# Optimization experiments

Hardware: AMD Instinct MI355X
Metric: run time of the kernel (lower is better)

Reference implementation:

```python
import jax, jax.numpy as jnp
import numpy as np

B, SQ, SKV, D, H, DH, P = 8, 2048, 2048, 1024, 8, 128, 1024
LN_EPS = 1e-3  # keras LayerNormalization default


def _glorot(key, shape):
    fan_in, fan_out = shape[-2], shape[-1]
    lim = np.sqrt(6.0 / (fan_in + fan_out))
    return jax.random.uniform(key, shape, jnp.float32, -lim, lim)


def _layernorm(x, gamma, beta, eps=LN_EPS):
    mu = jnp.mean(x, axis=-1, keepdims=True)
    var = jnp.mean(jnp.square(x - mu), axis=-1, keepdims=True)
    return (x - mu) * jax.lax.rsqrt(var + eps) * gamma + beta


def setup_inputs() -> dict:
    key = jax.random.key(0)
    ks = jax.random.split(key, 8)
    return {
        "query": jax.random.normal(ks[0], (B, SQ, D), jnp.float32),
        "value": jax.random.normal(ks[1], (B, SKV, D), jnp.float32),
        "W1": _glorot(ks[2], (H, D, DH)),   # per-head query proj (stacked)
        "W2": _glorot(ks[3], (H, D, DH)),   # per-head key proj
        "W3": _glorot(ks[4], (H, D, DH)),   # per-head value proj
        "Wp": _glorot(ks[5], (H * DH, P)),  # output projection
        "bp": jnp.zeros((P,), jnp.float32),
        "Wt": _glorot(ks[6], (P, P)),       # transform (relu FFN)
        "bt": jnp.zeros((P,), jnp.float32),
        "g1": jnp.ones((P,), jnp.float32),
        "b1": jnp.zeros((P,), jnp.float32),
        "g2": jnp.ones((P,), jnp.float32),
        "b2": jnp.zeros((P,), jnp.float32),
    }


def reference(query, value, W1, W2, W3, Wp, bp, Wt, bt, g1, b1, g2, b2):
    # batched multi-head attention (original loops over heads; math identical)
    q = jnp.einsum("bsd,hde->bhse", query, W1)   # [B,H,SQ,DH]
    k = jnp.einsum("btd,hde->bhte", value, W2)   # [B,H,SKV,DH]
    v = jnp.einsum("btd,hde->bhte", value, W3)   # [B,H,SKV,DH]
    scale = 1.0 / jnp.sqrt(jnp.asarray(DH, jnp.float32))
    scores = jnp.einsum("bhse,bhte->bhst", q, k) * scale
    attn = jax.nn.softmax(scores, axis=-1)
    ctx = jnp.einsum("bhst,bhte->bhse", attn, v)  # [B,H,SQ,DH]
    # concat heads along feature axis
    cat = ctx.transpose(0, 2, 1, 3).reshape(B, SQ, H * DH)
    # project + residual + layernorm (dropout inactive: rate=0 / inference)
    proj = cat @ Wp + bp + query
    proj = _layernorm(proj, g1, b1)
    # relu transform + residual + layernorm
    t = jax.nn.relu(proj @ Wt + bt) + proj
    return _layernorm(t, g2, b2)
```

## Files before the change

### kernel.cpp

```cpp
#include <hip/hip_runtime.h>
#include <hip/hip_bf16.h>


typedef __bf16 bf16x8 __attribute__((ext_vector_type(8)));
typedef float  f32x4  __attribute__((ext_vector_type(4)));
typedef float  f32x16 __attribute__((ext_vector_type(16)));
typedef unsigned u32x4 __attribute__((ext_vector_type(4)));

#define GLDS16(g, l)                                                         \
  __builtin_amdgcn_global_load_lds(                                          \
      (__attribute__((address_space(1))) void*)(g),                          \
      (__attribute__((address_space(3))) void*)(l), 16, 0, 0)

__device__ __forceinline__ unsigned short f2bfu(float f) {
  unsigned int u = __builtin_bit_cast(unsigned int, f);
  u += 0x7fffu + ((u >> 16) & 1u);
  return (unsigned short)(u >> 16);
}
__device__ __forceinline__ float bfu2f(unsigned short u) {
  return __builtin_bit_cast(float, (unsigned int)u << 16);
}

__global__ __launch_bounds__(256) void cast2_f32_bf16(
    const float* __restrict__ in0, unsigned short* __restrict__ out0,
    const float* __restrict__ in1, unsigned short* __restrict__ out1, int n) {
  const float* in = blockIdx.z ? in1 : in0;
  unsigned short* out = blockIdx.z ? out1 : out0;
  int i = (blockIdx.x * 256 + threadIdx.x) * 4;
  int stride = gridDim.x * 256 * 4;
  for (; i < n; i += stride) {
    float4 v = *(const float4*)(in + i);
    ushort4 o;
    o.x = f2bfu(v.x); o.y = f2bfu(v.y); o.z = f2bfu(v.z); o.w = f2bfu(v.w);
    *(ushort4*)(out + i) = o;
  }
}

__device__ __forceinline__ void tc_body(const float* in, unsigned short* out,
                                        int R, int C) {
  __shared__ float tile[32][33];
  int tx = threadIdx.x, ty = threadIdx.y;
  int c0 = blockIdx.x * 32, r0 = blockIdx.y * 32;
#pragma unroll
  for (int j = 0; j < 4; j++)
    tile[ty + j * 8][tx] = in[(size_t)(r0 + ty + j * 8) * C + c0 + tx];
  __syncthreads();
#pragma unroll
  for (int j = 0; j < 4; j++)
    out[(size_t)(c0 + ty + j * 8) * R + r0 + tx] = f2bfu(tile[tx][ty + j * 8]);
}

__global__ __launch_bounds__(256) void transpose_all(
    const float* __restrict__ W1, const float* __restrict__ W2,
    const float* __restrict__ W3, const float* __restrict__ Wp,
    const float* __restrict__ Wt, unsigned short* __restrict__ O1,
    unsigned short* __restrict__ O2, unsigned short* __restrict__ O3,
    unsigned short* __restrict__ Op, unsigned short* __restrict__ Ot) {
  int z = blockIdx.z;
  if (z < 24) {
    if (blockIdx.x >= 4) return;
    int t = z >> 3, s = z & 7;
    const float* in = (t == 0 ? W1 : t == 1 ? W2 : W3) + (size_t)s * 1024 * 128;
    unsigned short* out = (t == 0 ? O1 : t == 1 ? O2 : O3) + (size_t)s * 1024 * 128;
    tc_body(in, out, 1024, 128);
  } else {
    const float* in = (z == 24) ? Wp : Wt;
    unsigned short* out = (z == 24) ? Op : Ot;
    tc_body(in, out, 1024, 1024);
  }
}

__device__ __forceinline__ void gemm128_core(
    const char* gA, const char* gB, char* lds, f32x4 (&acc)[4][4], int tid) {
  int wid = tid >> 6, lane = tid & 63;
  int l15 = lane & 15, l4 = lane >> 4;
  int wm = (wid >> 1) * 64, wn = (wid & 1) * 64;

  auto STAGE = [&](int buf, int t) {
    char* ab = lds + buf * 32768;
    char* bb = ab + 16384;
#pragma unroll
    for (int i = 0; i < 4; i++) {
      int s = i * 256 + tid;
      int row = s >> 3;
      int g = (s & 7) ^ (row & 7);
      unsigned dst = (unsigned)((i * 256 + (tid & ~63)) * 16);
      GLDS16(gA + (size_t)row * 2048 + t * 128 + g * 16, ab + dst);
      GLDS16(gB + (size_t)row * 2048 + t * 128 + g * 16, bb + dst);
    }
  };

  STAGE(0, 0);
  for (int t = 0; t < 16; t++) {
    __builtin_amdgcn_sched_barrier(0);
    __builtin_amdgcn_s_barrier();
    if (t < 15) {
      STAGE((t + 1) & 1, t + 1);
      asm volatile("s_waitcnt vmcnt(8)" ::: "memory");
    } else {
      asm volatile("s_waitcnt vmcnt(0)" ::: "memory");
    }
    __builtin_amdgcn_s_barrier();
    __builtin_amdgcn_sched_barrier(0);

    const char* ab = lds + (t & 1) * 32768;
    const char* bb = ab + 16384;
#pragma unroll
    for (int kk = 0; kk < 2; kk++) {
      bf16x8 af[4], bfr[4];
#pragma unroll
      for (int f = 0; f < 4; f++) {
        int ra = wm + f * 16 + l15;
        af[f] = *(const bf16x8*)(ab + ra * 128 + (((kk * 4 + l4) ^ (ra & 7)) << 4));
        int rb = wn + f * 16 + l15;
        bfr[f] = *(const bf16x8*)(bb + rb * 128 + (((kk * 4 + l4) ^ (rb & 7)) << 4));
      }
      __builtin_amdgcn_s_setprio(1);
#pragma unroll
      for (int mf = 0; mf < 4; mf++)
#pragma unroll
        for (int nf = 0; nf < 4; nf++)
          acc[mf][nf] = __builtin_amdgcn_mfma_f32_16x16x32_bf16(
              af[mf], bfr[nf], acc[mf][nf], 0, 0, 0);
      __builtin_amdgcn_s_setprio(0);
    }
  }
}

__global__ __launch_bounds__(256, 2) void gemm_qkv(
    const unsigned short* __restrict__ qbf, const unsigned short* __restrict__ vbf,
    const unsigned short* __restrict__ Wq_t, const unsigned short* __restrict__ Wk_t,
    const unsigned short* __restrict__ Wv_t, unsigned short* __restrict__ Qh,
    unsigned short* __restrict__ Kh, unsigned short* __restrict__ Vt,
    float qscale) {
  int nb = gridDim.x;
  int qq = nb >> 3;
  int lin = blockIdx.x;
  int idx = (lin & 7) * qq + (lin >> 3);

  const unsigned short *A, *Bt;
  unsigned short* outp;
  int m0, n0, mode;
  float sc = 1.0f;
  if (idx < 2048) {
    int seg = idx >> 10;
    int t = idx & 1023;
    m0 = (t >> 3) * 128; n0 = (t & 7) * 128;
    A = seg ? vbf : qbf;
    Bt = seg ? Wk_t : Wq_t;
    outp = seg ? Kh : Qh;
    if (!seg) sc = qscale;
    mode = 0;
  } else {
    int v = idx - 2048;
    int bz = v >> 7, t = v & 127;
    m0 = (t >> 4) * 128; n0 = (t & 15) * 128;
    A = Wv_t;
    Bt = vbf + (size_t)bz * 2048 * 1024;
    outp = Vt + (size_t)bz * 1024 * 2048;
    mode = 1;
  }

  __shared__ alignas(16) char lds[65536];
  f32x4 acc[4][4];
#pragma unroll
  for (int i = 0; i < 4; i++)
#pragma unroll
    for (int j = 0; j < 4; j++) acc[i][j] = (f32x4){0.f, 0.f, 0.f, 0.f};

  gemm128_core((const char*)A + (size_t)m0 * 2048,
               (const char*)Bt + (size_t)n0 * 2048, lds, acc, threadIdx.x);

  int tid = threadIdx.x, wid = tid >> 6, lane = tid & 63;
  int l15 = lane & 15, l4 = lane >> 4;
  int wm = (wid >> 1) * 64, wn = (wid & 1) * 64;
#pragma unroll
  for (int mf = 0; mf < 4; mf++)
#pragma unroll
    for (int nf = 0; nf < 4; nf++)
#pragma unroll
      for (int r = 0; r < 4; r++) {
        int gm = m0 + wm + mf * 16 + l4 * 4 + r;
        int gn = n0 + wn + nf * 16 + l15;
        float v = acc[mf][nf][r];
        if (mode == 0) {
          int b = gm >> 11, s = gm & 2047, h = gn >> 7, e = gn & 127;
          outp[((((size_t)b * 8 + h) * 2048 + s) << 7) + e] = f2bfu(v * sc);
        } else {
          outp[(size_t)gm * 2048 + gn] = f2bfu(v);
        }
      }
}

template <int MODE>
__global__ __launch_bounds__(256, 2) void gemm128_ep(
    const unsigned short* __restrict__ A, const unsigned short* __restrict__ Bt,
    unsigned short* __restrict__ out, const float* __restrict__ bias,
    const unsigned short* __restrict__ extra) {
  int nb = gridDim.x;
  int qq = nb >> 3;
  int lin = blockIdx.x;
  int idx = (lin & 7) * qq + (lin >> 3);
  int m0 = (idx >> 3) * 128, n0 = (idx & 7) * 128;

  __shared__ alignas(16) char lds[65536];
  f32x4 acc[4][4];
#pragma unroll
  for (int i = 0; i < 4; i++)
#pragma unroll
    for (int j = 0; j < 4; j++) acc[i][j] = (f32x4){0.f, 0.f, 0.f, 0.f};

  gemm128_core((const char*)A + (size_t)m0 * 2048,
               (const char*)Bt + (size_t)n0 * 2048, lds, acc, threadIdx.x);

  int tid = threadIdx.x, wid = tid >> 6, lane = tid & 63;
  int l15 = lane & 15, l4 = lane >> 4;
  int wm = (wid >> 1) * 64, wn = (wid & 1) * 64;
#pragma unroll
  for (int mf = 0; mf < 4; mf++)
#pragma unroll
    for (int nf = 0; nf < 4; nf++)
#pragma unroll
      for (int r = 0; r < 4; r++) {
        int gm = m0 + wm + mf * 16 + l4 * 4 + r;
        int gn = n0 + wn + nf * 16 + l15;
        float v = acc[mf][nf][r];
        float pl = bfu2f(extra[(size_t)gm * 1024 + gn]);
        if constexpr (MODE == 2)
          out[(size_t)gm * 1024 + gn] = f2bfu(v + bias[gn] + pl);
        else
          out[(size_t)gm * 1024 + gn] = f2bfu(fmaxf(v + bias[gn], 0.0f) + pl);
      }
}

__global__ __launch_bounds__(512) void fa_kernel(
    const unsigned short* __restrict__ Qh,
    const unsigned short* __restrict__ Kh,
    const unsigned short* __restrict__ Vt,
    unsigned short* __restrict__ catO) {
  int h = blockIdx.x, qt = blockIdx.y, b = blockIdx.z;
  int tid = threadIdx.x, wid = tid >> 6, lane = tid & 63;
  int q31 = lane & 31, hi = lane >> 5;

  __shared__ alignas(16) char lds[131072];

  const char* gK = (const char*)(Kh + (((size_t)b * 8 + h) * 2048) * 128);
  const char* gV = (const char*)(Vt + ((size_t)b * 1024 + h * 128) * 2048);

  bf16x8 qf[8];
  {
    const char* gQ = (const char*)(Qh + (((size_t)b * 8 + h) * 2048
                        + (size_t)qt * 256 + wid * 32 + q31) * 128);
#pragma unroll
    for (int ks = 0; ks < 8; ks++)
      qf[ks] = *(const bf16x8*)(gQ + ks * 32 + hi * 16);
  }

  f32x16 o[4];
#pragma unroll
  for (int et = 0; et < 4; et++)
#pragma unroll
    for (int r = 0; r < 16; r++) o[et][r] = 0.f;
  float lacc0 = 0.f, lacc1 = 0.f;

  auto STAGE_K = [&](int kt) {
    char* kb = lds + (kt & 3) * 16384;
#pragma unroll
    for (int pass = 0; pass < 2; pass++) {
      int c = pass * 512 + tid;
      int row = c >> 4, ch = c & 15;
      int g = ch ^ (row & 15);
      GLDS16(gK + (size_t)(kt * 64 + row) * 256 + g * 16,
             kb + (pass * 512 + (tid & ~63)) * 16);
    }
  };
  auto STAGE_V = [&](int kt) {
    char* vb = lds + 65536 + (kt & 3) * 16384;
#pragma unroll
    for (int pass = 0; pass < 2; pass++) {
      int c = pass * 512 + tid;
      int row = c >> 4, g = c & 15;
      int gp = g ^ (row & 15);
      int e = ((gp >> 3) << 6) + row;
      GLDS16(gV + (size_t)e * 4096 + kt * 128 + (gp & 7) * 16,
             vb + (pass * 512 + (tid & ~63)) * 16);
    }
  };
  auto QK = [&](int kt, f32x16& r0, f32x16& r1) {
    const char* kb = lds + (kt & 3) * 16384;
#pragma unroll
    for (int r = 0; r < 16; r++) { r0[r] = 0.f; r1[r] = 0.f; }
#pragma unroll
    for (int ks = 0; ks < 8; ks++) {
      int g = ((2 * ks + hi) ^ (q31 & 15)) << 4;
      bf16x8 k0 = *(const bf16x8*)(kb + q31 * 256 + g);
      bf16x8 k1 = *(const bf16x8*)(kb + (q31 + 32) * 256 + g);
      r0 = __builtin_amdgcn_mfma_f32_32x32x16_bf16(k0, qf[ks], r0, 0, 0, 0);
      r1 = __builtin_amdgcn_mfma_f32_32x32x16_bf16(k1, qf[ks], r1, 0, 0, 0);
    }
  };
  auto SOFT_PV = [&](int kt, f32x16& s0, f32x16& s1) {
    float p[32];
#pragma unroll
    for (int r = 0; r < 16; r++) p[r] = __builtin_amdgcn_exp2f(s0[r]);
#pragma unroll
    for (int r = 0; r < 16; r++) p[16 + r] = __builtin_amdgcn_exp2f(s1[r]);
#pragma unroll
    for (int r = 0; r < 16; r++) { lacc0 += p[r]; lacc1 += p[16 + r]; }
    bf16x8 pa[4];
#pragma unroll
    for (int g = 0; g < 4; g++) {
      unsigned a0, a1, b0, b1;
      float p0 = p[g * 8 + 0], p1 = p[g * 8 + 1], p2 = p[g * 8 + 2], p3 = p[g * 8 + 3];
      float p4 = p[g * 8 + 4], p5 = p[g * 8 + 5], p6 = p[g * 8 + 6], p7 = p[g * 8 + 7];
      asm("v_cvt_pk_bf16_f32 %0, %1, %2" : "=v"(a0) : "v"(p0), "v"(p1));
      asm("v_cvt_pk_bf16_f32 %0, %1, %2" : "=v"(b0) : "v"(p4), "v"(p5));
      asm("v_cvt_pk_bf16_f32 %0, %1, %2" : "=v"(a1) : "v"(p2), "v"(p3));
      asm("v_cvt_pk_bf16_f32 %0, %1, %2" : "=v"(b1) : "v"(p6), "v"(p7));
      asm volatile("v_permlane32_swap_b32 %0, %1" : "+v"(a0), "+v"(b0));
      asm volatile("v_permlane32_swap_b32 %0, %1" : "+v"(a1), "+v"(b1));
      u32x4 w; w[0] = a0; w[1] = a1; w[2] = b0; w[3] = b1;
      pa[g] = __builtin_bit_cast(bf16x8, w);
    }
    const char* vb = lds + 65536 + (kt & 3) * 16384;
#pragma unroll
    for (int et = 0; et < 4; et++) {
      int row = (et & 1) * 32 + q31;
      int gb = (et >> 1) * 8;
#pragma unroll
      for (int ks = 0; ks < 4; ks++) {
        bf16x8 vf = *(const bf16x8*)(vb + row * 256 +
                        (((gb + 2 * ks + hi) ^ (row & 15)) << 4));
        o[et] = __builtin_amdgcn_mfma_f32_32x32x16_bf16(vf, pa[ks], o[et], 0, 0, 0);
      }
    }
  };

  STAGE_K(0); STAGE_V(0); STAGE_K(1); STAGE_V(1);

  for (int w = 0; w < 16; w++) {
    int kt = 2 * w;
    asm volatile("s_waitcnt lgkmcnt(0)" ::: "memory");
    __builtin_amdgcn_sched_barrier(0);
    __builtin_amdgcn_s_barrier();
    if (w < 15) {
      STAGE_K(kt + 2); STAGE_V(kt + 2); STAGE_K(kt + 3); STAGE_V(kt + 3);
      asm volatile("s_waitcnt vmcnt(8)" ::: "memory");
    } else {
      asm volatile("s_waitcnt vmcnt(0)" ::: "memory");
    }
    __builtin_amdgcn_s_barrier();
    __builtin_amdgcn_sched_barrier(0);
    f32x16 sA0, sA1, sB0, sB1;
    QK(kt, sA0, sA1);
    QK(kt + 1, sB0, sB1);
    SOFT_PV(kt, sA0, sA1);
    SOFT_PV(kt + 1, sB0, sB1);
  }

  float lacc = lacc0 + lacc1;
  lacc += __shfl_xor(lacc, 32);
  float linv = 1.0f / lacc;
  __syncthreads();
  char* reg = lds + wid * 8192;
  int swz = (lane & 7) << 4;
#pragma unroll
  for (int et = 0; et < 4; et++)
#pragma unroll
    for (int pr = 0; pr < 8; pr++) {
      float lo = o[et][2 * pr] * linv, hf = o[et][2 * pr + 1] * linv;
      unsigned w;
      asm("v_cvt_pk_bf16_f32 %0, %1, %2" : "=v"(w) : "v"(lo), "v"(hf));
      int e = et * 32 + 8 * (pr >> 1) + 4 * hi + (pr & 1) * 2;
      *(unsigned*)(reg + q31 * 256 + ((e * 2) ^ swz)) = w;
    }
  size_t orow = (size_t)b * 2048 + (size_t)qt * 256 + wid * 32;
#pragma unroll
  for (int pass = 0; pass < 8; pass++) {
    int n = pass * 64 + lane;
    int q = n >> 4, ch = n & 15;
    bf16x8 v = *(const bf16x8*)(reg + q * 256 + ((ch * 16) ^ ((q & 7) << 4)));
    *(bf16x8*)((char*)(catO + (orow + q) * 1024 + h * 128) + ch * 16) = v;
  }
}

template <int IN_BF16, int OUT_BF16>
__global__ __launch_bounds__(256) void ln_kernel(
    const void* __restrict__ in, const float* __restrict__ g,
    const float* __restrict__ be, void* __restrict__ out) {
  int row = blockIdx.x;
  int tid = threadIdx.x;
  float4 v;
  if constexpr (IN_BF16) {
    ushort4 u = ((const ushort4*)in)[(size_t)row * 256 + tid];
    v.x = bfu2f(u.x); v.y = bfu2f(u.y); v.z = bfu2f(u.z); v.w = bfu2f(u.w);
  } else {
    v = ((const float4*)in)[(size_t)row * 256 + tid];
  }
  float s = v.x + v.y + v.z + v.w;
  float sq = v.x * v.x + v.y * v.y + v.z * v.z + v.w * v.w;
#pragma unroll
  for (int m = 1; m < 64; m <<= 1) {
    s += __shfl_xor(s, m);
    sq += __shfl_xor(sq, m);
  }
  __shared__ float ws[8];
  int wid = tid >> 6, lane = tid & 63;
  if (lane == 0) { ws[wid] = s; ws[wid + 4] = sq; }
  __syncthreads();
  s = ws[0] + ws[1] + ws[2] + ws[3];
  sq = ws[4] + ws[5] + ws[6] + ws[7];
  float mu = s * (1.0f / 1024.0f);
  float var = sq * (1.0f / 1024.0f) - mu * mu;
  float rs = rsqrtf(var + 1e-3f);
  float4 gg = ((const float4*)g)[tid];
  float4 bb = ((const float4*)be)[tid];
  float y0 = (v.x - mu) * rs * gg.x + bb.x;
  float y1 = (v.y - mu) * rs * gg.y + bb.y;
  float y2 = (v.z - mu) * rs * gg.z + bb.z;
  float y3 = (v.w - mu) * rs * gg.w + bb.w;
  if constexpr (OUT_BF16) {
    ushort4 ov;
    ov.x = f2bfu(y0); ov.y = f2bfu(y1); ov.z = f2bfu(y2); ov.w = f2bfu(y3);
    ((ushort4*)out)[(size_t)row * 256 + tid] = ov;
  } else {
    float4 ov = {y0, y1, y2, y3};
    ((float4*)out)[(size_t)row * 256 + tid] = ov;
  }
}

extern "C" void kernel_launch(void* const* d_in, const int* in_sizes, int n_in,
                              void* d_out, int out_size, void* d_ws, size_t ws_size,
                              hipStream_t stream) {
  const float* query = (const float*)d_in[0];
  const float* value = (const float*)d_in[1];
  const float* W1 = (const float*)d_in[2];
  const float* W2 = (const float*)d_in[3];
  const float* W3 = (const float*)d_in[4];
  const float* Wp = (const float*)d_in[5];
  const float* bp = (const float*)d_in[6];
  const float* Wt = (const float*)d_in[7];
  const float* bt = (const float*)d_in[8];
  const float* g1 = (const float*)d_in[9];
  const float* b1 = (const float*)d_in[10];
  const float* g2 = (const float*)d_in[11];
  const float* b2 = (const float*)d_in[12];

  char* ws = (char*)d_ws;
  unsigned short* qbf  = (unsigned short*)(ws + 0);
  unsigned short* vbf  = (unsigned short*)(ws + 33554432);
  unsigned short* Qh   = (unsigned short*)(ws + 67108864);
  unsigned short* Kh   = (unsigned short*)(ws + 100663296);
  unsigned short* Vt   = (unsigned short*)(ws + 134217728);
  unsigned short* Wq_t = (unsigned short*)(ws + 167772160);
  unsigned short* Wk_t = (unsigned short*)(ws + 169869312);
  unsigned short* Wv_t = (unsigned short*)(ws + 171966464);
  unsigned short* Wp_t = (unsigned short*)(ws + 174063616);
  unsigned short* Wt_t = (unsigned short*)(ws + 176160768);
  unsigned short* cat_  = vbf;
  unsigned short* projb = Qh;
  unsigned short* pln   = vbf;
  unsigned short* tb    = Kh;

  const int NE = 16384 * 1024;
  cast2_f32_bf16<<<dim3(2048, 1, 2), 256, 0, stream>>>(query, qbf, value, vbf, NE);

  transpose_all<<<dim3(32, 32, 26), dim3(32, 8), 0, stream>>>(
      W1, W2, W3, Wp, Wt, Wq_t, Wk_t, Wv_t, Wp_t, Wt_t);

  const float QSCALE = 0.08838834764831845f * 1.4426950408889634f;
  gemm_qkv<<<3072, 256, 0, stream>>>(qbf, vbf, Wq_t, Wk_t, Wv_t, Qh, Kh, Vt, QSCALE);
  fa_kernel<<<dim3(8, 8, 8), 512, 0, stream>>>(Qh, Kh, Vt, cat_);
  gemm128_ep<2><<<1024, 256, 0, stream>>>(cat_, Wp_t, projb, bp, qbf);
  ln_kernel<1, 1><<<16384, 256, 0, stream>>>(projb, g1, b1, pln);
  gemm128_ep<3><<<1024, 256, 0, stream>>>(pln, Wt_t, tb, bt, pln);
  ln_kernel<1, 0><<<16384, 256, 0, stream>>>(tb, g2, b2, (float*)d_out);
}
```

Baseline: 414.1 us.

## Use 256x256 GEMM tiles with 512-thread blocks and fuse prep kernels

Enlarges the GEMM macro-tile from 128x128 to 256x256 with 8 waves per block, so each wave computes a 128x64 sub-tile, LDS grows to 128KB and grid sizes shrink four-fold. This is meant to raise operand reuse and cut global/LDS traffic per FLOP. It also fuses the input cast and weight transpose into a single launch to save launch overhead. The costs are more accumulator registers, likely only one block per CU given 128KB LDS, and fewer blocks (256 for the projection GEMMs) on a 256-CU device, which risks wave-quantization and lower latency hiding.

```diff
diff --git a/kernel.cpp b/kernel.cpp
--- a/kernel.cpp
+++ b/kernel.cpp
@@ -21,26 +21,10 @@
   return __builtin_bit_cast(float, (unsigned int)u << 16);
 }
 
-__global__ __launch_bounds__(256) void cast2_f32_bf16(
-    const float* __restrict__ in0, unsigned short* __restrict__ out0,
-    const float* __restrict__ in1, unsigned short* __restrict__ out1, int n) {
-  const float* in = blockIdx.z ? in1 : in0;
-  unsigned short* out = blockIdx.z ? out1 : out0;
-  int i = (blockIdx.x * 256 + threadIdx.x) * 4;
-  int stride = gridDim.x * 256 * 4;
-  for (; i < n; i += stride) {
-    float4 v = *(const float4*)(in + i);
-    ushort4 o;
-    o.x = f2bfu(v.x); o.y = f2bfu(v.y); o.z = f2bfu(v.z); o.w = f2bfu(v.w);
-    *(ushort4*)(out + i) = o;
-  }
-}
-
 __device__ __forceinline__ void tc_body(const float* in, unsigned short* out,
-                                        int R, int C) {
+                                        int R, int C, int c0, int r0,
+                                        int tx, int ty) {
   __shared__ float tile[32][33];
-  int tx = threadIdx.x, ty = threadIdx.y;
-  int c0 = blockIdx.x * 32, r0 = blockIdx.y * 32;
 #pragma unroll
   for (int j = 0; j < 4; j++)
     tile[ty + j * 8][tx] = in[(size_t)(r0 + ty + j * 8) * C + c0 + tx];
@@ -50,41 +34,60 @@
     out[(size_t)(c0 + ty + j * 8) * R + r0 + tx] = f2bfu(tile[tx][ty + j * 8]);
 }
 
-__global__ __launch_bounds__(256) void transpose_all(
+__global__ __launch_bounds__(256) void prep_fused(
+    const float* __restrict__ query, const float* __restrict__ value,
+    unsigned short* __restrict__ qbf, unsigned short* __restrict__ vbf,
     const float* __restrict__ W1, const float* __restrict__ W2,
     const float* __restrict__ W3, const float* __restrict__ Wp,
     const float* __restrict__ Wt, unsigned short* __restrict__ O1,
     unsigned short* __restrict__ O2, unsigned short* __restrict__ O3,
     unsigned short* __restrict__ Op, unsigned short* __restrict__ Ot) {
-  int z = blockIdx.z;
-  if (z < 24) {
-    if (blockIdx.x >= 4) return;
-    int t = z >> 3, s = z & 7;
+  int idx = blockIdx.x;
+  if (idx < 4096) {
+    const float* in = (idx < 2048) ? query : value;
+    unsigned short* out = (idx < 2048) ? qbf : vbf;
+    int blk = idx & 2047;
+    int i = (blk * 256 + threadIdx.x) * 4;
+    const int stride = 2048 * 256 * 4;
+    for (; i < 16777216; i += stride) {
+      float4 v = *(const float4*)(in + i);
+      ushort4 o;
+      o.x = f2bfu(v.x); o.y = f2bfu(v.y); o.z = f2bfu(v.z); o.w = f2bfu(v.w);
+      *(ushort4*)(out + i) = o;
+    }
+    return;
+  }
+  int t2 = idx - 4096;
+  int tx = threadIdx.x & 31, ty = threadIdx.x >> 5;
+  if (t2 < 3072) {
+    int slice = t2 >> 7, blk = t2 & 127;
+    int t = slice >> 3, s = slice & 7;
     const float* in = (t == 0 ? W1 : t == 1 ? W2 : W3) + (size_t)s * 1024 * 128;
     unsigned short* out = (t == 0 ? O1 : t == 1 ? O2 : O3) + (size_t)s * 1024 * 128;
-    tc_body(in, out, 1024, 128);
+    tc_body(in, out, 1024, 128, (blk & 3) * 32, (blk >> 2) * 32, tx, ty);
   } else {
-    const float* in = (z == 24) ? Wp : Wt;
-    unsigned short* out = (z == 24) ? Op : Ot;
-    tc_body(in, out, 1024, 1024);
-  }
-}
-
-__device__ __forceinline__ void gemm128_core(
-    const char* gA, const char* gB, char* lds, f32x4 (&acc)[4][4], int tid) {
+    int idx2 = t2 - 3072;
+    int zz = idx2 >> 10, blk = idx2 & 1023;
+    tc_body(zz ? Wt : Wp, zz ? Ot : Op, 1024, 1024,
+            (blk & 31) * 32, (blk >> 5) * 32, tx, ty);
+  }
+}
+
+__device__ __forceinline__ void gemm256_core(
+    const char* gA, const char* gB, char* lds, f32x4 (&acc)[8][4], int tid) {
   int wid = tid >> 6, lane = tid & 63;
   int l15 = lane & 15, l4 = lane >> 4;
-  int wm = (wid >> 1) * 64, wn = (wid & 1) * 64;
+  int wm = (wid >> 2) * 128, wn = (wid & 3) * 64;
 
   auto STAGE = [&](int buf, int t) {
-    char* ab = lds + buf * 32768;
-    char* bb = ab + 16384;
+    char* ab = lds + buf * 65536;
+    char* bb = ab + 32768;
 #pragma unroll
     for (int i = 0; i < 4; i++) {
-      int s = i * 256 + tid;
+      int s = i * 512 + tid;
       int row = s >> 3;
       int g = (s & 7) ^ (row & 7);
-      unsigned dst = (unsigned)((i * 256 + (tid & ~63)) * 16);
+      unsigned dst = (unsigned)((i * 512 + (tid & ~63)) * 16);
       GLDS16(gA + (size_t)row * 2048 + t * 128 + g * 16, ab + dst);
       GLDS16(gB + (size_t)row * 2048 + t * 128 + g * 16, bb + dst);
     }
@@ -103,31 +106,38 @@
     __builtin_amdgcn_s_barrier();
     __builtin_amdgcn_sched_barrier(0);
 
-    const char* ab = lds + (t & 1) * 32768;
-    const char* bb = ab + 16384;
+    const char* ab = lds + (t & 1) * 65536;
+    const char* bb = ab + 32768;
 #pragma unroll
     for (int kk = 0; kk < 2; kk++) {
-      bf16x8 af[4], bfr[4];
-#pragma unroll
-      for (int f = 0; f < 4; f++) {
-        int ra = wm + f * 16 + l15;
-        af[f] = *(const bf16x8*)(ab + ra * 128 + (((kk * 4 + l4) ^ (ra & 7)) << 4));
-        int rb = wn + f * 16 + l15;
-        bfr[f] = *(const bf16x8*)(bb + rb * 128 + (((kk * 4 + l4) ^ (rb & 7)) << 4));
+      bf16x8 bfr[4];
+#pragma unroll
+      for (int nf = 0; nf < 4; nf++) {
+        int r = wn + nf * 16 + l15;
+        bfr[nf] = *(const bf16x8*)(bb + r * 128 + (((kk * 4 + l4) ^ (r & 7)) << 4));
       }
-      __builtin_amdgcn_s_setprio(1);
-#pragma unroll
-      for (int mf = 0; mf < 4; mf++)
-#pragma unroll
-        for (int nf = 0; nf < 4; nf++)
-          acc[mf][nf] = __builtin_amdgcn_mfma_f32_16x16x32_bf16(
-              af[mf], bfr[nf], acc[mf][nf], 0, 0, 0);
-      __builtin_amdgcn_s_setprio(0);
-    }
-  }
-}
-
-__global__ __launch_bounds__(256, 2) void gemm_qkv(
+#pragma unroll
+      for (int mh = 0; mh < 2; mh++) {
+        bf16x8 af[4];
+#pragma unroll
+        for (int mf = 0; mf < 4; mf++) {
+          int r = wm + mh * 64 + mf * 16 + l15;
+          af[mf] = *(const bf16x8*)(ab + r * 128 + (((kk * 4 + l4) ^ (r & 7)) << 4));
+        }
+        __builtin_amdgcn_s_setprio(1);
+#pragma unroll
+        for (int mf = 0; mf < 4; mf++)
+#pragma unroll
+          for (int nf = 0; nf < 4; nf++)
+            acc[mh * 4 + mf][nf] = __builtin_amdgcn_mfma_f32_16x16x32_bf16(
+                af[mf], bfr[nf], acc[mh * 4 + mf][nf], 0, 0, 0);
+        __builtin_amdgcn_s_setprio(0);
+      }
+    }
+  }
+}
+
+__global__ __launch_bounds__(512, 2) void gemm_qkv(
     const unsigned short* __restrict__ qbf, const unsigned short* __restrict__ vbf,
     const unsigned short* __restrict__ Wq_t, const unsigned short* __restrict__ Wk_t,
     const unsigned short* __restrict__ Wv_t, unsigned short* __restrict__ Qh,
@@ -142,47 +152,47 @@
   unsigned short* outp;
   int m0, n0, mode;
   float sc = 1.0f;
-  if (idx < 2048) {
-    int seg = idx >> 10;
-    int t = idx & 1023;
-    m0 = (t >> 3) * 128; n0 = (t & 7) * 128;
+  if (idx < 512) {
+    int seg = idx >> 8;
+    int t = idx & 255;
+    m0 = (t >> 2) * 256; n0 = (t & 3) * 256;
     A = seg ? vbf : qbf;
     Bt = seg ? Wk_t : Wq_t;
     outp = seg ? Kh : Qh;
     if (!seg) sc = qscale;
     mode = 0;
   } else {
-    int v = idx - 2048;
-    int bz = v >> 7, t = v & 127;
-    m0 = (t >> 4) * 128; n0 = (t & 15) * 128;
+    int v = idx - 512;
+    int bz = v >> 5, t = v & 31;
+    m0 = (t >> 3) * 256; n0 = (t & 7) * 256;
     A = Wv_t;
     Bt = vbf + (size_t)bz * 2048 * 1024;
     outp = Vt + (size_t)bz * 1024 * 2048;
     mode = 1;
   }
 
-  __shared__ alignas(16) char lds[65536];
-  f32x4 acc[4][4];
-#pragma unroll
-  for (int i = 0; i < 4; i++)
+  __shared__ alignas(16) char lds[131072];
+  f32x4 acc[8][4];
+#pragma unroll
+  for (int i = 0; i < 8; i++)
 #pragma unroll
     for (int j = 0; j < 4; j++) acc[i][j] = (f32x4){0.f, 0.f, 0.f, 0.f};
 
-  gemm128_core((const char*)A + (size_t)m0 * 2048,
+  gemm256_core((const char*)A + (size_t)m0 * 2048,
                (const char*)Bt + (size_t)n0 * 2048, lds, acc, threadIdx.x);
 
   int tid = threadIdx.x, wid = tid >> 6, lane = tid & 63;
   int l15 = lane & 15, l4 = lane >> 4;
-  int wm = (wid >> 1) * 64, wn = (wid & 1) * 64;
-#pragma unroll
-  for (int mf = 0; mf < 4; mf++)
+  int wm = (wid >> 2) * 128, wn = (wid & 3) * 64;
+#pragma unroll
+  for (int mi = 0; mi < 8; mi++)
 #pragma unroll
     for (int nf = 0; nf < 4; nf++)
 #pragma unroll
       for (int r = 0; r < 4; r++) {
-        int gm = m0 + wm + mf * 16 + l4 * 4 + r;
+        int gm = m0 + wm + mi * 16 + l4 * 4 + r;
         int gn = n0 + wn + nf * 16 + l15;
-        float v = acc[mf][nf][r];
+        float v = acc[mi][nf][r];
         if (mode == 0) {
           int b = gm >> 11, s = gm & 2047, h = gn >> 7, e = gn & 127;
           outp[((((size_t)b * 8 + h) * 2048 + s) << 7) + e] = f2bfu(v * sc);
@@ -193,7 +203,7 @@
 }
 
 template <int MODE>
-__global__ __launch_bounds__(256, 2) void gemm128_ep(
+__global__ __launch_bounds__(512, 2) void gemm256_ep(
     const unsigned short* __restrict__ A, const unsigned short* __restrict__ Bt,
     unsigned short* __restrict__ out, const float* __restrict__ bias,
     const unsigned short* __restrict__ extra) {
@@ -201,30 +211,30 @@
   int qq = nb >> 3;
   int lin = blockIdx.x;
   int idx = (lin & 7) * qq + (lin >> 3);
-  int m0 = (idx >> 3) * 128, n0 = (idx & 7) * 128;
-
-  __shared__ alignas(16) char lds[65536];
-  f32x4 acc[4][4];
-#pragma unroll
-  for (int i = 0; i < 4; i++)
+  int m0 = (idx >> 2) * 256, n0 = (idx & 3) * 256;
+
+  __shared__ alignas(16) char lds[131072];
+  f32x4 acc[8][4];
+#pragma unroll
+  for (int i = 0; i < 8; i++)
 #pragma unroll
     for (int j = 0; j < 4; j++) acc[i][j] = (f32x4){0.f, 0.f, 0.f, 0.f};
 
-  gemm128_core((const char*)A + (size_t)m0 * 2048,
+  gemm256_core((const char*)A + (size_t)m0 * 2048,
                (const char*)Bt + (size_t)n0 * 2048, lds, acc, threadIdx.x);
 
   int tid = threadIdx.x, wid = tid >> 6, lane = tid & 63;
   int l15 = lane & 15, l4 = lane >> 4;
-  int wm = (wid >> 1) * 64, wn = (wid & 1) * 64;
-#pragma unroll
-  for (int mf = 0; mf < 4; mf++)
+  int wm = (wid >> 2) * 128, wn = (wid & 3) * 64;
+#pragma unroll
+  for (int mi = 0; mi < 8; mi++)
 #pragma unroll
     for (int nf = 0; nf < 4; nf++)
 #pragma unroll
       for (int r = 0; r < 4; r++) {
-        int gm = m0 + wm + mf * 16 + l4 * 4 + r;
+        int gm = m0 + wm + mi * 16 + l4 * 4 + r;
         int gn = n0 + wn + nf * 16 + l15;
-        float v = acc[mf][nf][r];
+        float v = acc[mi][nf][r];
         float pl = bfu2f(extra[(size_t)gm * 1024 + gn]);
         if constexpr (MODE == 2)
           out[(size_t)gm * 1024 + gn] = f2bfu(v + bias[gn] + pl);
@@ -462,17 +472,16 @@
   unsigned short* pln   = vbf;
   unsigned short* tb    = Kh;
 
-  const int NE = 16384 * 1024;
-  cast2_f32_bf16<<<dim3(2048, 1, 2), 256, 0, stream>>>(query, qbf, value, vbf, NE);
-
-  transpose_all<<<dim3(32, 32, 26), dim3(32, 8), 0, stream>>>(
-      W1, W2, W3, Wp, Wt, Wq_t, Wk_t, Wv_t, Wp_t, Wt_t);
+  prep_fused<<<9216, 256, 0, stream>>>(query, value, qbf, vbf,
+                                       W1, W2, W3, Wp, Wt,
+                                       Wq_t, Wk_t, Wv_t, Wp_t, Wt_t);
 
   const float QSCALE = 0.08838834764831845f * 1.4426950408889634f;
-  gemm_qkv<<<3072, 256, 0, stream>>>(qbf, vbf, Wq_t, Wk_t, Wv_t, Qh, Kh, Vt, QSCALE);
+  gemm_qkv<<<768, 512, 0, stream>>>(qbf, vbf, Wq_t, Wk_t, Wv_t,
+                                    Qh, Kh, Vt, QSCALE);
   fa_kernel<<<dim3(8, 8, 8), 512, 0, stream>>>(Qh, Kh, Vt, cat_);
-  gemm128_ep<2><<<1024, 256, 0, stream>>>(cat_, Wp_t, projb, bp, qbf);
+  gemm256_ep<2><<<256, 512, 0, stream>>>(cat_, Wp_t, projb, bp, qbf);
   ln_kernel<1, 1><<<16384, 256, 0, stream>>>(projb, g1, b1, pln);
-  gemm128_ep<3><<<1024, 256, 0, stream>>>(pln, Wt_t, tb, bt, pln);
+  gemm256_ep<3><<<256, 512, 0, stream>>>(pln, Wt_t, tb, bt, pln);
   ln_kernel<1, 0><<<16384, 256, 0, stream>>>(tb, g2, b2, (float*)d_out);
 }
```

Result: faster. 398.1 us (-3.9%).
